# Kernel tuning notes

Hardware: AMD Instinct MI355X
Metric: run time of the kernel (lower is better)

Reference implementation:

```python
import jax, jax.numpy as jnp
import numpy as np


def setup_inputs() -> dict:
    key = jax.random.key(0)
    k1, k2, k3 = jax.random.split(key, 3)
    B, N, M, S = 2, 8192, 32768, 4096
    pred = jax.random.normal(k1, (B, N, 3), dtype=jnp.float32)
    target = jax.random.normal(k2, (B, M, 3), dtype=jnp.float32)
    # stands in for torch.randperm(N)[:S]; duplicates don't change the math shape-wise
    idx = jax.random.randint(k3, (S,), 0, N, dtype=jnp.int64)
    return {"pred": pred, "target": target, "idx": idx}


def reference(pred, target, idx):
    # pred: (B, N, 3), target: (B, M, 3), idx: (S,)
    pred_s = pred[:, idx, :]                       # (B, S, 3) -- sampled points
    x2 = jnp.sum(pred_s * pred_s, axis=-1)         # (B, S)
    y2 = jnp.sum(target * target, axis=-1)         # (B, M)
    xy = jnp.einsum("bsd,bmd->bsm", pred_s, target)  # (B, S, M)
    d2 = x2[:, :, None] + y2[:, None, :] - 2.0 * xy
    dist = jnp.sqrt(jnp.maximum(d2, 0.0))          # (B, S, M)
    min_dist = jnp.min(dist, axis=2)               # (B, S)
    return jnp.mean(min_dist)
```

## Files before the change

### kernel.cpp

```cpp
#include <hip/hip_runtime.h>
#include <math.h>

constexpr int B = 2;
constexpr int N = 8192;
constexpr int M = 32768;
constexpr int S = 4096;
constexpr int QTOT = B * S;
constexpr int R = 16;
constexpr int WT = 64 * R;
constexpr int TCH = M / WT;
constexpr int QG = S / 64;
constexpr int WAVES = B * TCH * QG;
constexpr int BLOCKS = WAVES / 4;


__global__ __launch_bounds__(256) void chamfer_prep(
    const float* __restrict__ pred, const int* __restrict__ idx,
    float4* __restrict__ qrec, unsigned* __restrict__ wsmin) {
  int q = blockIdx.x * 256 + threadIdx.x;
  if (q >= QTOT) return;
  int b = q / S;
  int s = q - b * S;
  int i = idx[s];
  const float* p = pred + ((size_t)b * N + (size_t)i) * 3;
  float x = p[0], y = p[1], z = p[2];
  qrec[q] = make_float4(-2.0f * x, -2.0f * y, -2.0f * z,
                        x * x + y * y + z * z);
  wsmin[q] = 0x7F800000u;
}

__global__ __launch_bounds__(256) void chamfer_main(
    const float* __restrict__ target, const float4* __restrict__ qrec,
    unsigned* __restrict__ wsmin) {
  const int lane = threadIdx.x & 63;
  const int w = blockIdx.x * 4 + (threadIdx.x >> 6);
  const int b = w >> 11;
  const int rem = w & 2047;
  const int tch = rem & (TCH - 1);
  const int qg = rem >> 5;

  const float* tb = target + ((size_t)b * M + (size_t)tch * WT) * 3;
  float t0[R], t1[R], t2[R], ty2[R];
#pragma unroll
  for (int j = 0; j < R; ++j) {
    int m = j * 64 + lane;
    float a = tb[3 * m + 0];
    float c = tb[3 * m + 1];
    float d = tb[3 * m + 2];
    t0[j] = a; t1[j] = c; t2[j] = d;
    ty2[j] = fmaf(a, a, fmaf(c, c, d * d));
  }

  const int q = b * S + qg * 64 + lane;
  float4 qr = qrec[q];
  float q0 = qr.x, q1 = qr.y, q2 = qr.z, qx2 = qr.w;
  float m0 = INFINITY, m1 = INFINITY;

  for (int step = 0; step < 64; ++step) {
#pragma unroll
    for (int j = 0; j < R; j += 2) {
      float s0 = qx2 + ty2[j];
      s0 = fmaf(q0, t0[j], s0);
      s0 = fmaf(q1, t1[j], s0);
      s0 = fmaf(q2, t2[j], s0);
      m0 = fminf(m0, s0);
      float s1 = qx2 + ty2[j + 1];
      s1 = fmaf(q0, t0[j + 1], s1);
      s1 = fmaf(q1, t1[j + 1], s1);
      s1 = fmaf(q2, t2[j + 1], s1);
      m1 = fminf(m1, s1);
    }
    float mm = fminf(m0, m1);
    int src = (lane + 1) & 63;
    q0 = __shfl(q0, src);
    q1 = __shfl(q1, src);
    q2 = __shfl(q2, src);
    qx2 = __shfl(qx2, src);
    mm = __shfl(mm, src);
    m0 = mm;
    m1 = INFINITY;
  }
  float mm = fminf(m0, m1);
  mm = fmaxf(mm, 0.0f);
  atomicMin(&wsmin[q], __float_as_uint(mm));
}

__global__ __launch_bounds__(256) void chamfer_finish(
    const unsigned* __restrict__ wsmin, float* __restrict__ out) {
  float sum = 0.0f;
  for (int q = threadIdx.x; q < QTOT; q += 256)
    sum += sqrtf(__uint_as_float(wsmin[q]));
#pragma unroll
  for (int off = 32; off > 0; off >>= 1)
    sum += __shfl_down(sum, off, 64);
  __shared__ float red[4];
  int wv = threadIdx.x >> 6;
  if ((threadIdx.x & 63) == 0) red[wv] = sum;
  __syncthreads();
  if (threadIdx.x == 0) {
    out[0] = (red[0] + red[1] + red[2] + red[3]) / (float)QTOT;
  }
}

extern "C" void kernel_launch(void* const* d_in, const int* in_sizes, int n_in,
                              void* d_out, int out_size, void* d_ws, size_t ws_size,
                              hipStream_t stream) {
  const float* pred = (const float*)d_in[0];
  const float* target = (const float*)d_in[1];
  const int* idx = (const int*)d_in[2];
  unsigned* wsmin = (unsigned*)d_ws;
  float4* qrec = (float4*)((char*)d_ws + 32 * 1024);

  chamfer_prep<<<QTOT / 256, 256, 0, stream>>>(pred, idx, qrec, wsmin);
  chamfer_main<<<BLOCKS, 256, 0, stream>>>(target, qrec, wsmin);
  chamfer_finish<<<1, 256, 0, stream>>>(wsmin, (float*)d_out);
}
```

Measured before the change: 95.49 us.

## Use packed fp32 FMAs, LDS-broadcast queries, hoisted query norm in chamfer main loop

The inner distance loop now pairs two target points into 2-wide float vectors so the compiler can emit packed fp32 FMAs. The per-query squared norm is moved out of the loop and added once at the end, which is valid because adding a constant does not change which value is the minimum. Query records are staged in shared memory and read by a rotating index, so each step needs one ds_bpermute for the running minimum instead of five shuffles. The finish kernel grows to 1024 threads. In exchange the kernel adds a shared-memory load and a block barrier, and it depends on the compiler actually emitting packed instructions.

New measurement: 84.50 us. -11.5%, faster.

```diff
diff --git a/kernel.cpp b/kernel.cpp
--- a/kernel.cpp
+++ b/kernel.cpp
@@ -1,5 +1,7 @@
 #include <hip/hip_runtime.h>
 #include <math.h>
+
+typedef float vf2 __attribute__((ext_vector_type(2)));
 
 constexpr int B = 2;
 constexpr int N = 8192;
@@ -32,6 +34,7 @@
 __global__ __launch_bounds__(256) void chamfer_main(
     const float* __restrict__ target, const float4* __restrict__ qrec,
     unsigned* __restrict__ wsmin) {
+  __shared__ float4 qs[64];
   const int lane = threadIdx.x & 63;
   const int w = blockIdx.x * 4 + (threadIdx.x >> 6);
   const int b = w >> 11;
@@ -39,66 +42,70 @@
   const int tch = rem & (TCH - 1);
   const int qg = rem >> 5;
 
+  if (threadIdx.x < 64)
+    qs[threadIdx.x] = qrec[b * S + qg * 64 + threadIdx.x];
+
   const float* tb = target + ((size_t)b * M + (size_t)tch * WT) * 3;
-  float t0[R], t1[R], t2[R], ty2[R];
+  vf2 t0p[8], t1p[8], t2p[8], ty2p[8];
 #pragma unroll
-  for (int j = 0; j < R; ++j) {
-    int m = j * 64 + lane;
-    float a = tb[3 * m + 0];
-    float c = tb[3 * m + 1];
-    float d = tb[3 * m + 2];
-    t0[j] = a; t1[j] = c; t2[j] = d;
-    ty2[j] = fmaf(a, a, fmaf(c, c, d * d));
+  for (int p = 0; p < 8; ++p) {
+    int mA = (2 * p) * 64 + lane;
+    int mB = (2 * p + 1) * 64 + lane;
+    float ax = tb[3 * mA], ay = tb[3 * mA + 1], az = tb[3 * mA + 2];
+    float bx = tb[3 * mB], by = tb[3 * mB + 1], bz = tb[3 * mB + 2];
+    t0p[p] = vf2{ax, bx};
+    t1p[p] = vf2{ay, by};
+    t2p[p] = vf2{az, bz};
+    ty2p[p] = vf2{fmaf(ax, ax, fmaf(ay, ay, az * az)),
+                  fmaf(bx, bx, fmaf(by, by, bz * bz))};
   }
+  __syncthreads();
 
-  const int q = b * S + qg * 64 + lane;
-  float4 qr = qrec[q];
-  float q0 = qr.x, q1 = qr.y, q2 = qr.z, qx2 = qr.w;
-  float m0 = INFINITY, m1 = INFINITY;
+  const float qx2_home = qs[lane].w;
+  const int rot = ((lane + 1) & 63) * 4;
+  float mm = INFINITY;
+  int qoff = lane;
 
   for (int step = 0; step < 64; ++step) {
+    float4 qr = qs[qoff];
+    vf2 q0 = vf2{qr.x, qr.x}, q1 = vf2{qr.y, qr.y}, q2 = vf2{qr.z, qr.z};
+    float m0 = mm, m1 = INFINITY;
 #pragma unroll
-    for (int j = 0; j < R; j += 2) {
-      float s0 = qx2 + ty2[j];
-      s0 = fmaf(q0, t0[j], s0);
-      s0 = fmaf(q1, t1[j], s0);
-      s0 = fmaf(q2, t2[j], s0);
-      m0 = fminf(m0, s0);
-      float s1 = qx2 + ty2[j + 1];
-      s1 = fmaf(q0, t0[j + 1], s1);
-      s1 = fmaf(q1, t1[j + 1], s1);
-      s1 = fmaf(q2, t2[j + 1], s1);
-      m1 = fminf(m1, s1);
+    for (int p = 0; p < 8; p += 2) {
+      vf2 s = __builtin_elementwise_fma(q0, t0p[p], ty2p[p]);
+      s = __builtin_elementwise_fma(q1, t1p[p], s);
+      s = __builtin_elementwise_fma(q2, t2p[p], s);
+      m0 = fminf(fminf(s.x, s.y), m0);
+      vf2 u = __builtin_elementwise_fma(q0, t0p[p + 1], ty2p[p + 1]);
+      u = __builtin_elementwise_fma(q1, t1p[p + 1], u);
+      u = __builtin_elementwise_fma(q2, t2p[p + 1], u);
+      m1 = fminf(fminf(u.x, u.y), m1);
     }
-    float mm = fminf(m0, m1);
-    int src = (lane + 1) & 63;
-    q0 = __shfl(q0, src);
-    q1 = __shfl(q1, src);
-    q2 = __shfl(q2, src);
-    qx2 = __shfl(qx2, src);
-    mm = __shfl(mm, src);
-    m0 = mm;
-    m1 = INFINITY;
+    mm = fminf(m0, m1);
+    mm = __int_as_float(__builtin_amdgcn_ds_bpermute(rot, __float_as_int(mm)));
+    qoff = (qoff + 1) & 63;
   }
-  float mm = fminf(m0, m1);
-  mm = fmaxf(mm, 0.0f);
-  atomicMin(&wsmin[q], __float_as_uint(mm));
+  const int q = b * S + qg * 64 + lane;
+  atomicMin(&wsmin[q], __float_as_uint(fmaxf(qx2_home + mm, 0.0f)));
 }
 
-__global__ __launch_bounds__(256) void chamfer_finish(
+__global__ __launch_bounds__(1024) void chamfer_finish(
     const unsigned* __restrict__ wsmin, float* __restrict__ out) {
+  __shared__ float red[16];
   float sum = 0.0f;
-  for (int q = threadIdx.x; q < QTOT; q += 256)
+  for (int q = threadIdx.x; q < QTOT; q += 1024)
     sum += sqrtf(__uint_as_float(wsmin[q]));
 #pragma unroll
   for (int off = 32; off > 0; off >>= 1)
     sum += __shfl_down(sum, off, 64);
-  __shared__ float red[4];
   int wv = threadIdx.x >> 6;
   if ((threadIdx.x & 63) == 0) red[wv] = sum;
   __syncthreads();
   if (threadIdx.x == 0) {
-    out[0] = (red[0] + red[1] + red[2] + red[3]) / (float)QTOT;
+    float t = 0.0f;
+#pragma unroll
+    for (int i = 0; i < 16; ++i) t += red[i];
+    out[0] = t / (float)QTOT;
   }
 }
 
@@ -113,5 +120,5 @@
 
   chamfer_prep<<<QTOT / 256, 256, 0, stream>>>(pred, idx, qrec, wsmin);
   chamfer_main<<<BLOCKS, 256, 0, stream>>>(target, qrec, wsmin);
-  chamfer_finish<<<1, 256, 0, stream>>>(wsmin, (float*)d_out);
+  chamfer_finish<<<1, 1024, 0, stream>>>(wsmin, (float*)d_out);
 }
```
